# Kernel tuning notes

Hardware: AMD Instinct MI355X
Metric: run time of the kernel (lower is better)

Reference implementation:

```python
import jax, jax.numpy as jnp
import numpy as np

LAMBDA_E_SUM = 10.0
LAMBDA_HIT = 20.0
LAMBDA_CHAMFER = 1e-3
LAMBDA_HIT_ENTROPY = 0.1
EPS = 1e-6
BIG = 1e18


def setup_inputs() -> dict:
    key = jax.random.key(0)
    ks = jax.random.split(key, 7)
    B, Np, Ng, L = 32, 2048, 2048, 256
    pred_feat = jax.random.normal(ks[0], (B, 4, Np), dtype=jnp.float32)
    # hit-probability channel must be in (0,1) (sigmoid head in the real model)
    pred_hit = jax.random.uniform(ks[1], (B, 1, Np), dtype=jnp.float32,
                                  minval=1e-4, maxval=1.0 - 1e-4)
    preds = jnp.concatenate([pred_feat, pred_hit], axis=1)          # [B,5,Np]
    target = jax.random.normal(ks[2], (B, 4, Ng), dtype=jnp.float32)  # [B,4,Ng]
    target_mask = (jax.random.uniform(ks[3], (B, Ng)) < 0.9).astype(jnp.float32)
    mu = jax.random.normal(ks[4], (B, L), dtype=jnp.float32)
    logvar = 0.5 * jax.random.normal(ks[5], (B, L), dtype=jnp.float32)
    e_init = jax.random.uniform(ks[6], (B,), dtype=jnp.float32,
                                minval=10.0, maxval=100.0)
    kl_weight = jnp.float32(1e-3)
    return {"preds": preds, "target": target, "target_mask": target_mask,
            "mu": mu, "logvar": logvar, "e_init": e_init,
            "kl_weight": kl_weight}


def reference(preds, target, target_mask, mu, logvar, e_init, kl_weight):
    B = preds.shape[0]
    preds_t = jnp.swapaxes(preds, 1, 2)    # [B, Np, 5]
    target_t = jnp.swapaxes(target, 1, 2)  # [B, Ng, 4]
    pred_xyz = preds_t[..., :3]            # [B, Np, 3]
    pred_E = preds_t[..., 3]               # [B, Np]
    pred_hit = preds_t[..., 4]             # [B, Np]
    target_xyz = target_t[..., :3]         # [B, Ng, 3]
    target_E = target_t[..., 3]            # [B, Ng]

    # squared pairwise distances [B, Np, Ng]
    pn = jnp.sum(pred_xyz * pred_xyz, axis=-1)      # [B, Np]
    tn = jnp.sum(target_xyz * target_xyz, axis=-1)  # [B, Ng]
    dist_sq = jnp.maximum(
        pn[:, :, None] + tn[:, None, :]
        - 2.0 * jnp.einsum('bnd,bmd->bnm', pred_xyz, target_xyz), 0.0)

    inf_mask = target_mask[:, None, :] == 0.0       # [B, 1->Np, Ng]
    dist_sq_masked = jnp.where(inf_mask, BIG, dist_sq)
    min_dist_pred = jnp.min(dist_sq_masked, axis=2)     # [B, Np]
    idx_pred = jnp.argmin(dist_sq_masked, axis=2)       # [B, Np]
    min_dist_target = jnp.min(dist_sq, axis=1)          # [B, Ng]

    mask_sum = jnp.sum(target_mask)
    loss_chamfer_target = jnp.sum(min_dist_target * target_mask) / mask_sum
    loss_chamfer_pred = jnp.mean(min_dist_pred)
    loss_chamfer = loss_chamfer_target + loss_chamfer_pred

    matched_target_E = jnp.take_along_axis(target_E, idx_pred, axis=1)  # [B, Np]
    loss_local_E = jnp.mean(jnp.abs(pred_E - matched_target_E))

    n_hits_pred = jnp.sum(pred_hit, axis=1)                 # [B]
    n_hits_target = jnp.sum(target_mask, axis=1)            # [B]
    loss_hit_count = jnp.mean((n_hits_pred - n_hits_target) ** 2)

    loss_hit_entropy = -jnp.mean(pred_hit * jnp.log(pred_hit + EPS)
                                 + (1.0 - pred_hit) * jnp.log(1.0 - pred_hit + EPS))

    total_pred_E = jnp.sum(pred_E * pred_hit, axis=1)       # [B]
    loss_global_E_sum = jnp.mean((total_pred_E - e_init) ** 2)

    loss_kld = -0.5 * jnp.sum(1.0 + logvar - mu * mu - jnp.exp(logvar)) / B

    loss_chamf = loss_chamfer * LAMBDA_CHAMFER
    losskld = kl_weight * loss_kld
    loss_global_e = LAMBDA_E_SUM * loss_global_E_sum
    loss_hit = LAMBDA_HIT * loss_hit_count
    loss_hit_entr = LAMBDA_HIT_ENTROPY * loss_hit_entropy

    total_loss = (loss_chamf + loss_local_E + losskld
                  + loss_global_e + loss_hit + loss_hit_entr)
    components = jnp.stack([loss_chamf, loss_local_E, loss_global_e,
                            loss_hit, losskld])
    return total_loss, components
```

## Files before the change

kernel.cpp:

```cpp
#include <hip/hip_runtime.h>

#define BB 32
#define NP 2048
#define NG 2048
#define EPSF 1e-6f
#define BIGF 1e18f
#define FLTMAX 3.4e38f
#define MT 128
#define MP 16
#define TPT 8

#define FPART_OFF 0
#define PPART_OFF 65536
#define TPART_OFF (65536 + BB * MP * NP * 8)

__global__ __launch_bounds__(256, 8) void k_pair(const float* __restrict__ preds,
                                                 const float* __restrict__ target,
                                                 const float* __restrict__ mask,
                                                 unsigned long long* __restrict__ ppart,
                                                 float* __restrict__ tpart) {
  __shared__ float4 s4[MT];
  const int bx = blockIdx.x;
  const int tid = threadIdx.x;

  if (bx < 512) {
    const int b = bx >> 4;
    const int mp = bx & 15;
    const float* tb = target + b * 4 * NG;
    const int mbase = mp * MT;
    if (tid < MT) {
      int m = mbase + tid;
      float tx = tb[m], ty = tb[NG + m], tz = tb[2 * NG + m];
      float tn = fmaf(tx, tx, fmaf(ty, ty, tz * tz));
      float w = tn + (mask[b * NG + m] == 0.0f ? BIGF : 0.0f);
      s4[tid] = make_float4(-2.0f * tx, -2.0f * ty, -2.0f * tz, w);
    }
    __syncthreads();

    const float* pb = preds + b * 5 * NP;
    float px[TPT], py[TPT], pz[TPT], bv[TPT];
    int bi[TPT];
#pragma unroll
    for (int k = 0; k < TPT; k++) {
      int n = tid + k * 256;
      px[k] = pb[n];
      py[k] = pb[NP + n];
      pz[k] = pb[2 * NP + n];
      bv[k] = FLTMAX;
      bi[k] = 0;
    }

#pragma unroll 2
    for (int m = 0; m < MT; m++) {
      float4 t = s4[m];
#pragma unroll
      for (int k = 0; k < TPT; k++) {
        float s = fmaf(px[k], t.x, fmaf(py[k], t.y, fmaf(pz[k], t.z, t.w)));
        if (s < bv[k]) { bv[k] = s; bi[k] = m; }
      }
    }

    unsigned long long* row = &ppart[(b * MP + mp) * NP];
#pragma unroll
    for (int k = 0; k < TPT; k++) {
      float pn = fmaf(px[k], px[k], fmaf(py[k], py[k], pz[k] * pz[k]));
      float d = fmaxf(bv[k] + pn, 0.0f);
      row[tid + k * 256] =
          ((unsigned long long)__float_as_uint(d) << 32) | (unsigned)(mbase + bi[k]);
    }
  } else {
    const int bb = bx - 512;
    const int b = bb >> 4;
    const int np_ = bb & 15;
    const float* pb = preds + b * 5 * NP;
    if (tid < MT) {
      int n = np_ * MT + tid;
      float px = pb[n], py = pb[NP + n], pz = pb[2 * NP + n];
      float pn2 = fmaf(px, px, fmaf(py, py, pz * pz));
      s4[tid] = make_float4(-2.0f * px, -2.0f * py, -2.0f * pz, pn2);
    }
    __syncthreads();

    const float* tb = target + b * 4 * NG;
    float tx[TPT], ty[TPT], tz[TPT], cv[TPT];
#pragma unroll
    for (int k = 0; k < TPT; k++) {
      int m = tid + k * 256;
      tx[k] = tb[m];
      ty[k] = tb[NG + m];
      tz[k] = tb[2 * NG + m];
      cv[k] = FLTMAX;
    }

#pragma unroll 2
    for (int n = 0; n < MT; n++) {
      float4 p = s4[n];
#pragma unroll
      for (int k = 0; k < TPT; k++)
        cv[k] = fminf(cv[k], fmaf(tx[k], p.x, fmaf(ty[k], p.y, fmaf(tz[k], p.z, p.w))));
    }

    float* row = &tpart[(b * MP + np_) * NG];
#pragma unroll
    for (int k = 0; k < TPT; k++) {
      float tn = fmaf(tx[k], tx[k], fmaf(ty[k], ty[k], tz[k] * tz[k]));
      row[tid + k * 256] = fmaxf(cv[k] + tn, 0.0f);
    }
  }
}

__global__ __launch_bounds__(256) void k_fin(const unsigned long long* __restrict__ ppart,
                                             const float* __restrict__ tpart,
                                             const float* __restrict__ preds,
                                             const float* __restrict__ target,
                                             const float* __restrict__ mask,
                                             const float* __restrict__ mu,
                                             const float* __restrict__ logvar,
                                             float* __restrict__ fpart) {
  __shared__ float red[4][8];
  const int bx = blockIdx.x;
  const int tid = threadIdx.x;
  const int wave = tid >> 6, lane = tid & 63;
  float q0 = 0.0f, q1 = 0.0f, q2 = 0.0f, q3 = 0.0f, q4 = 0.0f;

  if (bx < 128) {
    const int b = bx >> 2;
    const float* pb = preds + b * 5 * NP;
    const float* te = target + b * 4 * NG + 3 * NG;
#pragma unroll
    for (int e = 0; e < 2; e++) {
      int i = bx * 512 + e * 256 + tid;
      int n = i & 2047;
      unsigned long long best = 0xFFFFFFFFFFFFFFFFull;
      const unsigned long long* col = &ppart[b * MP * NP + n];
#pragma unroll
      for (int mp = 0; mp < MP; mp++) {
        unsigned long long v = col[mp * NP];
        best = v < best ? v : best;
      }
      float bd = __uint_as_float((unsigned)(best >> 32));
      int idx = (int)(best & 0xffffffffu);
      float mE = te[idx];
      float pE = pb[3 * NP + n];
      float ph = pb[4 * NP + n];
      q0 += bd;
      q1 += fabsf(pE - mE);
      q2 += ph * logf(ph + EPSF) + (1.0f - ph) * logf(1.0f - ph + EPSF);
      q3 += ph;
      q4 += pE * ph;
    }
  } else if (bx < 256) {
    const int bb = bx - 128;
    const int b = bb >> 2;
#pragma unroll
    for (int e = 0; e < 2; e++) {
      int i = bb * 512 + e * 256 + tid;
      int m = i & 2047;
      float d = FLTMAX;
      const float* col = &tpart[b * MP * NG + m];
#pragma unroll
      for (int np_ = 0; np_ < MP; np_++) d = fminf(d, col[np_ * NG]);
      float msk = mask[i];
      q0 += d * msk;
      q1 += msk;
      q2 += msk;
    }
  } else {
    const int bb = bx - 256;
#pragma unroll
    for (int e = 0; e < 4; e++) {
      int i = bb * 1024 + e * 256 + tid;
      float m = mu[i], lv = logvar[i];
      q0 += 1.0f + lv - m * m - expf(lv);
    }
  }

  float qs[5] = {q0, q1, q2, q3, q4};
  for (int k = 0; k < 5; k++) {
    float v = qs[k];
    v += __shfl_down(v, 32);
    v += __shfl_down(v, 16);
    v += __shfl_down(v, 8);
    v += __shfl_down(v, 4);
    v += __shfl_down(v, 2);
    v += __shfl_down(v, 1);
    if (lane == 0) red[wave][k] = v;
  }
  __syncthreads();
  if (tid < 5) fpart[bx * 8 + tid] = red[0][tid] + red[1][tid] + red[2][tid] + red[3][tid];
}

__global__ __launch_bounds__(256) void k_final(const float* __restrict__ fpart,
                                               const float* __restrict__ e_init,
                                               const float* __restrict__ kl_weight,
                                               float* __restrict__ out) {
  __shared__ float red[4][8];
  const int t = threadIdx.x;
  const int wave = t >> 6, lane = t & 63;
  float g[8] = {0, 0, 0, 0, 0, 0, 0, 0};
  if (t < 128) {
    const float* r = &fpart[t * 8];
    g[0] = r[0]; g[1] = r[1]; g[2] = r[2];
    const float* r2 = &fpart[(128 + t) * 8];
    g[3] = r2[0]; g[4] = r2[1];
  }
  if (t < 8) g[5] = fpart[(256 + t) * 8];
  if (t < BB) {
    float hit = 0.0f, eh = 0.0f, mk = 0.0f;
#pragma unroll
    for (int k = 0; k < 4; k++) {
      hit += fpart[(4 * t + k) * 8 + 3];
      eh += fpart[(4 * t + k) * 8 + 4];
      mk += fpart[(128 + 4 * t + k) * 8 + 2];
    }
    float dh = hit - mk;
    g[6] = dh * dh;
    float de = eh - e_init[t];
    g[7] = de * de;
  }
  for (int k = 0; k < 8; k++) {
    float v = g[k];
    v += __shfl_down(v, 32);
    v += __shfl_down(v, 16);
    v += __shfl_down(v, 8);
    v += __shfl_down(v, 4);
    v += __shfl_down(v, 2);
    v += __shfl_down(v, 1);
    if (lane == 0) red[wave][k] = v;
  }
  __syncthreads();
  if (t == 0) {
    float s[8];
    for (int k = 0; k < 8; k++) s[k] = red[0][k] + red[1][k] + red[2][k] + red[3][k];
    const float invBN = 1.0f / (float)(BB * NP);
    float chamfer_pred = s[0] * invBN;
    float localE = s[1] * invBN;
    float ent = -s[2] * invBN;
    float chamfer_tgt = s[3] / s[4];
    float kld = -0.5f * s[5] / (float)BB;
    float hit = s[6] / (float)BB;
    float ge = s[7] / (float)BB;

    float loss_chamf = (chamfer_tgt + chamfer_pred) * 0.001f;
    float losskld = kl_weight[0] * kld;
    float loss_ge = 10.0f * ge;
    float loss_hit = 20.0f * hit;
    float loss_ent = 0.1f * ent;

    float total = loss_chamf + localE + losskld + loss_ge + loss_hit + loss_ent;
    out[0] = total;
    out[1] = loss_chamf;
    out[2] = localE;
    out[3] = loss_ge;
    out[4] = loss_hit;
    out[5] = losskld;
  }
}

extern "C" void kernel_launch(void* const* d_in, const int* in_sizes, int n_in,
                              void* d_out, int out_size, void* d_ws, size_t ws_size,
                              hipStream_t stream) {
  const float* preds = (const float*)d_in[0];
  const float* target = (const float*)d_in[1];
  const float* mask = (const float*)d_in[2];
  const float* mu = (const float*)d_in[3];
  const float* logvar = (const float*)d_in[4];
  const float* e_init = (const float*)d_in[5];
  const float* kl_weight = (const float*)d_in[6];
  float* fpart = (float*)((char*)d_ws + FPART_OFF);
  unsigned long long* ppart = (unsigned long long*)((char*)d_ws + PPART_OFF);
  float* tpart = (float*)((char*)d_ws + TPART_OFF);
  float* out = (float*)d_out;

  k_pair<<<1024, 256, 0, stream>>>(preds, target, mask, ppart, tpart);
  k_fin<<<264, 256, 0, stream>>>(ppart, tpart, preds, target, mask, mu, logvar, fpart);
  k_final<<<1, 256, 0, stream>>>(fpart, e_init, kl_weight, out);
}
```

Baseline: 105.6 us.

## Compute pairwise distances with bf16 MFMA tiles and fuse both chamfer directions

Replaces the two separate scalar FMA passes (pred→target and target→pred) with a single kernel that computes 16x16 distance tiles using bf16 MFMA instructions, encoding norms and mask as extra K entries. Each tile feeds both the row-wise argmin and column-wise min, then partial results are reduced via shuffles and LDS. This cuts VALU work per pair and halves the distance computation. The trade-off is bf16 precision, which may change nearest-neighbor indices and distances relative to the fp32 reference.

```diff
diff --git a/kernel.cpp b/kernel.cpp
--- a/kernel.cpp
+++ b/kernel.cpp
@@ -6,106 +6,130 @@
 #define EPSF 1e-6f
 #define BIGF 1e18f
 #define FLTMAX 3.4e38f
-#define MT 128
-#define MP 16
-#define TPT 8
+#define MPP 8
+#define MPT 32
+
+typedef float f32x4 __attribute__((ext_vector_type(4)));
+typedef short s16x8 __attribute__((ext_vector_type(8)));
 
 #define FPART_OFF 0
 #define PPART_OFF 65536
-#define TPART_OFF (65536 + BB * MP * NP * 8)
-
-__global__ __launch_bounds__(256, 8) void k_pair(const float* __restrict__ preds,
+#define TPART_OFF (65536 + BB * MPP * NP * 8)
+
+__device__ __forceinline__ unsigned short f2bf(float f) {
+  unsigned x = __float_as_uint(f);
+  unsigned r = x + 0x7fffu + ((x >> 16) & 1u);
+  return (unsigned short)(r >> 16);
+}
+
+__global__ __launch_bounds__(256, 8) void k_dist(const float* __restrict__ preds,
                                                  const float* __restrict__ target,
                                                  const float* __restrict__ mask,
                                                  unsigned long long* __restrict__ ppart,
                                                  float* __restrict__ tpart) {
-  __shared__ float4 s4[MT];
+  __shared__ unsigned long long tS[256];
+  __shared__ float cmw[256][4];
   const int bx = blockIdx.x;
+  const int b = bx >> 8;
+  const int R = (bx >> 3) & 31;
+  const int C = bx & 7;
   const int tid = threadIdx.x;
-
-  if (bx < 512) {
-    const int b = bx >> 4;
-    const int mp = bx & 15;
+  const int w = tid >> 6;
+  const int l = tid & 63;
+  const int lm = l & 15;
+  const int quad = l >> 4;
+  const int c0 = C * 256;
+  const int r0 = R * 64;
+
+  {
+    const int n = c0 + tid;
     const float* tb = target + b * 4 * NG;
-    const int mbase = mp * MT;
-    if (tid < MT) {
-      int m = mbase + tid;
-      float tx = tb[m], ty = tb[NG + m], tz = tb[2 * NG + m];
-      float tn = fmaf(tx, tx, fmaf(ty, ty, tz * tz));
-      float w = tn + (mask[b * NG + m] == 0.0f ? BIGF : 0.0f);
-      s4[tid] = make_float4(-2.0f * tx, -2.0f * ty, -2.0f * tz, w);
-    }
-    __syncthreads();
-
+    float tx = tb[n], ty = tb[NG + n], tz = tb[2 * NG + n];
+    float tn = fmaf(tx, tx, fmaf(ty, ty, tz * tz));
+    float w3 = (mask[b * NG + n] == 0.0f) ? BIGF : tn;
+    unsigned long long pk =
+        (unsigned long long)f2bf(-2.0f * tx) |
+        ((unsigned long long)f2bf(-2.0f * ty) << 16) |
+        ((unsigned long long)f2bf(-2.0f * tz) << 32) |
+        ((unsigned long long)f2bf(w3) << 48);
+    tS[tid] = pk;
+  }
+
+  s16x8 afrag = {0, 0, 0, 0, 0, 0, 0, 0};
+  {
+    const int row = r0 + 16 * w + lm;
     const float* pb = preds + b * 5 * NP;
-    float px[TPT], py[TPT], pz[TPT], bv[TPT];
-    int bi[TPT];
-#pragma unroll
-    for (int k = 0; k < TPT; k++) {
-      int n = tid + k * 256;
-      px[k] = pb[n];
-      py[k] = pb[NP + n];
-      pz[k] = pb[2 * NP + n];
-      bv[k] = FLTMAX;
-      bi[k] = 0;
-    }
-
-#pragma unroll 2
-    for (int m = 0; m < MT; m++) {
-      float4 t = s4[m];
-#pragma unroll
-      for (int k = 0; k < TPT; k++) {
-        float s = fmaf(px[k], t.x, fmaf(py[k], t.y, fmaf(pz[k], t.z, t.w)));
-        if (s < bv[k]) { bv[k] = s; bi[k] = m; }
-      }
-    }
-
-    unsigned long long* row = &ppart[(b * MP + mp) * NP];
-#pragma unroll
-    for (int k = 0; k < TPT; k++) {
-      float pn = fmaf(px[k], px[k], fmaf(py[k], py[k], pz[k] * pz[k]));
-      float d = fmaxf(bv[k] + pn, 0.0f);
-      row[tid + k * 256] =
-          ((unsigned long long)__float_as_uint(d) << 32) | (unsigned)(mbase + bi[k]);
-    }
-  } else {
-    const int bb = bx - 512;
-    const int b = bb >> 4;
-    const int np_ = bb & 15;
-    const float* pb = preds + b * 5 * NP;
-    if (tid < MT) {
-      int n = np_ * MT + tid;
-      float px = pb[n], py = pb[NP + n], pz = pb[2 * NP + n];
-      float pn2 = fmaf(px, px, fmaf(py, py, pz * pz));
-      s4[tid] = make_float4(-2.0f * px, -2.0f * py, -2.0f * pz, pn2);
-    }
-    __syncthreads();
-
-    const float* tb = target + b * 4 * NG;
-    float tx[TPT], ty[TPT], tz[TPT], cv[TPT];
-#pragma unroll
-    for (int k = 0; k < TPT; k++) {
-      int m = tid + k * 256;
-      tx[k] = tb[m];
-      ty[k] = tb[NG + m];
-      tz[k] = tb[2 * NG + m];
-      cv[k] = FLTMAX;
-    }
-
-#pragma unroll 2
-    for (int n = 0; n < MT; n++) {
-      float4 p = s4[n];
-#pragma unroll
-      for (int k = 0; k < TPT; k++)
-        cv[k] = fminf(cv[k], fmaf(tx[k], p.x, fmaf(ty[k], p.y, fmaf(tz[k], p.z, p.w))));
-    }
-
-    float* row = &tpart[(b * MP + np_) * NG];
-#pragma unroll
-    for (int k = 0; k < TPT; k++) {
-      float tn = fmaf(tx[k], tx[k], fmaf(ty[k], ty[k], tz[k] * tz[k]));
-      row[tid + k * 256] = fmaxf(cv[k] + tn, 0.0f);
-    }
+    float px = pb[row], py = pb[NP + row], pz = pb[2 * NP + row];
+    float pn = fmaf(px, px, fmaf(py, py, pz * pz));
+    if (quad == 0) {
+      afrag[0] = (short)f2bf(px);
+      afrag[1] = (short)f2bf(py);
+      afrag[2] = (short)f2bf(pz);
+      afrag[3] = (short)0x3f80;
+      afrag[4] = (short)f2bf(pn);
+    }
+  }
+  __syncthreads();
+
+  float bv[4] = {FLTMAX, FLTMAX, FLTMAX, FLTMAX};
+  int bi[4] = {0, 0, 0, 0};
+  float cv[16];
+
+#pragma unroll
+  for (int t = 0; t < 16; t++) {
+    unsigned long long pk = tS[t * 16 + lm];
+    s16x8 bfrag = {0, 0, 0, 0, 0, 0, 0, 0};
+    if (quad == 0) {
+      bfrag[0] = (short)(pk & 0xffffu);
+      bfrag[1] = (short)((pk >> 16) & 0xffffu);
+      bfrag[2] = (short)((pk >> 32) & 0xffffu);
+      bfrag[3] = (short)(pk >> 48);
+      bfrag[4] = (short)0x3f80;
+    }
+    f32x4 acc = {0.0f, 0.0f, 0.0f, 0.0f};
+    acc = __builtin_amdgcn_mfma_f32_16x16x32_bf16(afrag, bfrag, acc, 0, 0, 0);
+#pragma unroll
+    for (int r = 0; r < 4; r++) {
+      if (acc[r] < bv[r]) { bv[r] = acc[r]; bi[r] = t * 16 + lm; }
+    }
+    cv[t] = fminf(fminf(acc[0], acc[1]), fminf(acc[2], acc[3]));
+  }
+
+#pragma unroll
+  for (int off = 1; off < 16; off <<= 1) {
+#pragma unroll
+    for (int r = 0; r < 4; r++) {
+      float ov = __shfl_xor(bv[r], off);
+      int oi = __shfl_xor(bi[r], off);
+      if (ov < bv[r] || (ov == bv[r] && oi < bi[r])) { bv[r] = ov; bi[r] = oi; }
+    }
+  }
+  if (lm == 0) {
+    unsigned long long* prow = &ppart[(b * MPP + C) * NP];
+#pragma unroll
+    for (int r = 0; r < 4; r++) {
+      int grow = r0 + 16 * w + quad * 4 + r;
+      float d = fmaxf(bv[r], 0.0f);
+      prow[grow] = ((unsigned long long)__float_as_uint(d) << 32) | (unsigned)(c0 + bi[r]);
+    }
+  }
+
+#pragma unroll
+  for (int t = 0; t < 16; t++) {
+    float v = cv[t];
+    v = fminf(v, __shfl_xor(v, 16));
+    v = fminf(v, __shfl_xor(v, 32));
+    cv[t] = v;
+  }
+  if (quad == 0) {
+#pragma unroll
+    for (int t = 0; t < 16; t++) cmw[t * 16 + lm][w] = cv[t];
+  }
+  __syncthreads();
+  {
+    float4 m4 = *(const float4*)cmw[tid];
+    float cm = fminf(fminf(m4.x, m4.y), fminf(m4.z, m4.w));
+    tpart[(b * MPT + R) * NG + c0 + tid] = fmaxf(cm, 0.0f);
   }
 }
 
@@ -132,9 +156,9 @@
       int i = bx * 512 + e * 256 + tid;
       int n = i & 2047;
       unsigned long long best = 0xFFFFFFFFFFFFFFFFull;
-      const unsigned long long* col = &ppart[b * MP * NP + n];
-#pragma unroll
-      for (int mp = 0; mp < MP; mp++) {
+      const unsigned long long* col = &ppart[b * MPP * NP + n];
+#pragma unroll
+      for (int mp = 0; mp < MPP; mp++) {
         unsigned long long v = col[mp * NP];
         best = v < best ? v : best;
       }
@@ -157,9 +181,9 @@
       int i = bb * 512 + e * 256 + tid;
       int m = i & 2047;
       float d = FLTMAX;
-      const float* col = &tpart[b * MP * NG + m];
-#pragma unroll
-      for (int np_ = 0; np_ < MP; np_++) d = fminf(d, col[np_ * NG]);
+      const float* col = &tpart[b * MPT * NG + m];
+#pragma unroll
+      for (int np_ = 0; np_ < MPT; np_++) d = fminf(d, col[np_ * NG]);
       float msk = mask[i];
       q0 += d * msk;
       q1 += msk;
@@ -272,7 +296,7 @@
   float* tpart = (float*)((char*)d_ws + TPART_OFF);
   float* out = (float*)d_out;
 
-  k_pair<<<1024, 256, 0, stream>>>(preds, target, mask, ppart, tpart);
+  k_dist<<<BB * 32 * 8, 256, 0, stream>>>(preds, target, mask, ppart, tpart);
   k_fin<<<264, 256, 0, stream>>>(ppart, tpart, preds, target, mask, mu, logvar, fpart);
   k_final<<<1, 256, 0, stream>>>(fpart, e_init, kl_weight, out);
 }
```

Measured after the change: 152.2 us. 44.1% more time.
